# Performance work log

Hardware: AMD Instinct MI355X
Metric: run time of the kernel (lower is better)

The kernel has to match this reference:

```python
import jax, jax.numpy as jnp
import numpy as np

T, B, D, W = 1024, 8, 512, 32

def setup_inputs() -> dict:
    key = jax.random.key(0)
    k1, k2, k3 = jax.random.split(key, 3)
    inputs = jax.random.normal(k1, (T, B, D), dtype=jnp.float32)
    weight_W = jax.random.uniform(k2, (D, D), dtype=jnp.float32, minval=-0.1, maxval=0.1)
    weight_proj = jax.random.uniform(k3, (D, 1), dtype=jnp.float32, minval=-0.1, maxval=0.1)
    return {"inputs": inputs, "weight_W": weight_W, "weight_proj": weight_proj,
            "attention_width": W}

def reference(inputs, weight_W, weight_proj, attention_width):
    # inputs: [T, B, D]. For step i < w: passthrough. For i >= w: attend over
    # window inputs[i-w : i] (current step EXCLUDED, matching the original).
    Tn, Bn, Dn = inputs.shape
    w = attention_width
    # window gather indices: row t corresponds to output step i = t + w,
    # covering timesteps [i-w, i) == [t, t+w)
    idx = jnp.arange(Tn - w)[:, None] + jnp.arange(w)          # [T-w, w]
    windows = inputs[idx]                                       # [T-w, w, B, D]
    u = jnp.tanh(jnp.einsum('twbd,de->twbe', windows, weight_W))  # [T-w, w, B, D]
    scores = jnp.einsum('twbd,d->twb', u, weight_proj[:, 0])      # [T-w, w, B]
    # NOTE: original uses legacy nn.Softmax() on a [w, B] tensor, whose implicit
    # dim is 1 (the batch dim). We reproduce that math faithfully: softmax over B.
    a = jax.nn.softmax(scores, axis=-1)                           # [T-w, w, B]
    attended = jnp.einsum('twb,twbd->tbd', a, windows)            # [T-w, B, D]
    return jnp.concatenate([inputs[:w], attended], axis=0)       # [T, B, D]
```

## Files before the change

### kernel.cpp

```cpp
#include <hip/hip_runtime.h>
#include <cstdint>

namespace {
constexpr int T = 1024;
constexpr int B = 8;
constexpr int D = 512;
constexpr int W = 32;
constexpr int M = T * B;
}

using half8  = __attribute__((ext_vector_type(8))) _Float16;
using f32x16 = __attribute__((ext_vector_type(16))) float;

__device__ __forceinline__ void gload16(const void* g, void* l) {
    __builtin_amdgcn_global_load_lds(
        (const __attribute__((address_space(1))) void*)g,
        (__attribute__((address_space(3))) void*)l, 16, 0, 0);
}

__device__ __forceinline__ float fast_tanh(float x) {
    float e = __expf(2.f * x);
    return 1.f - 2.f / (e + 1.f);
}

__global__ __launch_bounds__(256) void prep_merged(
    const float* __restrict__ X, const float* __restrict__ Wm,
    _Float16* __restrict__ Ah, _Float16* __restrict__ Bt)
{
    __shared__ float tile[64][65];
    const int tid = threadIdx.x;
    const int bid = blockIdx.x;

    {
        const int c = bid * 256 + tid;
        const float4* X4 = reinterpret_cast<const float4*>(X);
        const float4 v0 = X4[(size_t)c * 2];
        const float4 v1 = X4[(size_t)c * 2 + 1];
        half8 h;
        h[0] = (_Float16)v0.x; h[1] = (_Float16)v0.y; h[2] = (_Float16)v0.z; h[3] = (_Float16)v0.w;
        h[4] = (_Float16)v1.x; h[5] = (_Float16)v1.y; h[6] = (_Float16)v1.z; h[7] = (_Float16)v1.w;
        *reinterpret_cast<half8*>(Ah + (size_t)c * 8) = h;
    }

    if (bid < 64) {
        const int bd = bid & 7;
        const int be = bid >> 3;
        const int r  = tid >> 2;
        const int c0 = (tid & 3) * 16;
        const float* src = Wm + (size_t)(be * 64 + r) * 512 + bd * 64 + c0;
#pragma unroll
        for (int j = 0; j < 16; j += 4) {
            const float4 v = *reinterpret_cast<const float4*>(src + j);
            tile[r][c0 + j]     = v.x;
            tile[r][c0 + j + 1] = v.y;
            tile[r][c0 + j + 2] = v.z;
            tile[r][c0 + j + 3] = v.w;
        }
        __syncthreads();
        const int dd = tid >> 2;
        const int e0 = (tid & 3) * 16;
        half8 h0, h1;
#pragma unroll
        for (int j = 0; j < 8; ++j)  h0[j] = (_Float16)tile[e0 + j][dd];
#pragma unroll
        for (int j = 0; j < 8; ++j)  h1[j] = (_Float16)tile[e0 + 8 + j][dd];
        _Float16* dst = Bt + (size_t)(bd * 64 + dd) * 512 + be * 64 + e0;
        *reinterpret_cast<half8*>(dst)     = h0;
        *reinterpret_cast<half8*>(dst + 8) = h1;
    }
}

__global__ __launch_bounds__(256) void gemm_scores(
    const _Float16* __restrict__ Ah, const _Float16* __restrict__ Bt,
    const float* __restrict__ proj, float* __restrict__ spart)
{
    __shared__ char lds_buf[49152];

    const int tid  = threadIdx.x;
    const int lane = tid & 63;
    const int wv   = tid >> 6;
    const int wm   = wv >> 1;
    const int wn   = wv & 1;
    const int hi   = lane >> 5;
    const int l31  = lane & 31;
    const int l7   = lane & 7;

    const int bid  = blockIdx.x;
    const int wgid = (bid & 7) * 64 + (bid >> 3);
    const int mb   = wgid >> 2;
    const int nb   = wgid & 3;
    const int m0   = mb * 64;
    const int n0   = nb * 128;

    const int wbase = __builtin_amdgcn_readfirstlane(tid & ~63);

    f32x16 acc0 = {}, acc1 = {};

    auto stage = [&](int bufi, int kt) {
        char* abase = lds_buf + bufi * 24576;
        char* bbase = abase + 8192;
        const int kbase = kt * 64;
#pragma unroll
        for (int i = 0; i < 2; ++i) {
            const int c   = i * 256 + tid;
            const int row = c >> 3;
            const int ch  = c & 7;
            const int koff = kbase + ((ch ^ (row & 7)) << 3);
            gload16(Ah + (size_t)(m0 + row) * 512 + koff,
                    abase + (size_t)(i * 256 + wbase) * 16);
        }
#pragma unroll
        for (int i = 0; i < 4; ++i) {
            const int c   = i * 256 + tid;
            const int row = c >> 3;
            const int ch  = c & 7;
            const int koff = kbase + ((ch ^ (row & 7)) << 3);
            gload16(Bt + (size_t)(n0 + row) * 512 + koff,
                    bbase + (size_t)(i * 256 + wbase) * 16);
        }
    };

    stage(0, 0);
    asm volatile("s_waitcnt vmcnt(0)" ::: "memory");
    __syncthreads();

    int cur = 0;
    const int rowA  = wm * 32 + l31;
    const int colB0 = wn * 64 + l31;
    const int colB1 = colB0 + 32;

    for (int kt = 0; kt < 8; ++kt) {
        if (kt < 7) stage(cur ^ 1, kt + 1);

        const char* Ab = lds_buf + cur * 24576;
        const char* Bb = Ab + 8192;

        half8 af[4], bf0[4], bf1[4];
#pragma unroll
        for (int s = 0; s < 4; ++s) {
            const int ch = ((2 * s + hi) ^ l7) << 4;
            af[s]  = *reinterpret_cast<const half8*>(Ab + rowA  * 128 + ch);
            bf0[s] = *reinterpret_cast<const half8*>(Bb + colB0 * 128 + ch);
            bf1[s] = *reinterpret_cast<const half8*>(Bb + colB1 * 128 + ch);
        }
        __builtin_amdgcn_s_setprio(1);
#pragma unroll
        for (int s = 0; s < 4; ++s) {
            acc0 = __builtin_amdgcn_mfma_f32_32x32x16_f16(af[s], bf0[s], acc0, 0, 0, 0);
            acc1 = __builtin_amdgcn_mfma_f32_32x32x16_f16(af[s], bf1[s], acc1, 0, 0, 0);
        }
        __builtin_amdgcn_s_setprio(0);

        if (kt < 7) asm volatile("s_waitcnt vmcnt(0)" ::: "memory");
        __syncthreads();
        cur ^= 1;
    }

    const float pj0 = proj[n0 + wn * 64 + l31];
    const float pj1 = proj[n0 + wn * 64 + 32 + l31];
    float* sp = spart + (size_t)(nb * 2 + wn) * M;

#pragma unroll
    for (int reg = 0; reg < 16; ++reg) {
        float v0 = fast_tanh(acc0[reg]) * pj0 + fast_tanh(acc1[reg]) * pj1;
#pragma unroll
        for (int msk = 1; msk < 32; msk <<= 1)
            v0 += __shfl_xor(v0, msk, 64);
        if (l31 == 0) {
            const int rl = (reg & 3) + 8 * (reg >> 2) + 4 * hi;
            sp[m0 + wm * 32 + rl] = v0;
        }
    }
}

__global__ __launch_bounds__(256) void attend_kernel(
    const float* __restrict__ X, const _Float16* __restrict__ Ah,
    const float* __restrict__ spart, float* __restrict__ out)
{
    __shared__ _Float16 W_lds[63 * 512];
    __shared__ float p_lds[64];

    const int bid = blockIdx.x;
    const int b   = bid & 7;
    const int ig  = bid >> 3;
    const int tid = threadIdx.x;

    if (ig == 0) {
        const float4* X4 = reinterpret_cast<const float4*>(X);
        float4* O4 = reinterpret_cast<float4*>(out);
        for (int idx = tid; idx < 32 * 128; idx += 256) {
            const int r = idx >> 7;
            const int c = idx & 127;
            const size_t off = (size_t)(r * 8 + b) * 128 + c;
            O4[off] = X4[off];
        }
        return;
    }

    const int i0   = ig * 32;
    const int tau0 = i0 - 32;
    const int lane = tid & 63;
    const int wbase = __builtin_amdgcn_readfirstlane(tid & ~63);

    {
        const _Float16* src = Ah + (size_t)(tau0 * 8 + b) * 512;
#pragma unroll
        for (int it = 0; it < 16; ++it) {
            const int cbase = it * 256 + wbase;
            if (cbase < 4032) {
                const int c  = cbase + lane;
                const int r  = c >> 6;
                const int ch = c & 63;
                gload16(src + (size_t)r * 4096 + ch * 8,
                        (char*)W_lds + (size_t)cbase * 16);
            }
        }
    }

    const int bj = tid & 7;
#pragma unroll
    for (int half = 0; half < 2; ++half) {
        const int lt = (tid >> 3) + half * 32;
        if (lt < 63) {
            float s = 0.f;
#pragma unroll
            for (int g = 0; g < 8; ++g)
                s += spart[(size_t)g * M + (size_t)(tau0 + lt) * 8 + bj];
            float mx = s;
#pragma unroll
            for (int msk = 1; msk < 8; msk <<= 1)
                mx = fmaxf(mx, __shfl_xor(mx, msk, 64));
            const float e = __expf(s - mx);
            float sum = e;
#pragma unroll
            for (int msk = 1; msk < 8; msk <<= 1)
                sum += __shfl_xor(sum, msk, 64);
            if (bj == b) p_lds[lt] = e / sum;
        }
    }

    asm volatile("s_waitcnt vmcnt(0)" ::: "memory");
    __syncthreads();

    const int rg = tid >> 6;

#pragma unroll 2
    for (int q = 0; q < 8; ++q) {
        const int i  = i0 + rg * 8 + q;
        const int lb = rg * 8 + q;
        float a0 = 0.f, a1 = 0.f, a2 = 0.f, a3 = 0.f;
        float a4 = 0.f, a5 = 0.f, a6 = 0.f, a7 = 0.f;
#pragma unroll 4
        for (int k = 0; k < 32; ++k) {
            const int lt = lb + k;
            const float pw = p_lds[lt];
            const half8 h = *reinterpret_cast<const half8*>(
                W_lds + (size_t)lt * 512 + lane * 8);
            a0 = fmaf(pw, (float)h[0], a0);
            a1 = fmaf(pw, (float)h[1], a1);
            a2 = fmaf(pw, (float)h[2], a2);
            a3 = fmaf(pw, (float)h[3], a3);
            a4 = fmaf(pw, (float)h[4], a4);
            a5 = fmaf(pw, (float)h[5], a5);
            a6 = fmaf(pw, (float)h[6], a6);
            a7 = fmaf(pw, (float)h[7], a7);
        }
        float4* O4 = reinterpret_cast<float4*>(
            out + (size_t)(i * 8 + b) * 512 + lane * 8);
        O4[0] = float4{a0, a1, a2, a3};
        O4[1] = float4{a4, a5, a6, a7};
    }
}

extern "C" void kernel_launch(void* const* d_in, const int* in_sizes, int n_in,
                              void* d_out, int out_size, void* d_ws, size_t ws_size,
                              hipStream_t stream)
{
    const float* X    = (const float*)d_in[0];
    const float* Wm   = (const float*)d_in[1];
    const float* proj = (const float*)d_in[2];
    float* out = (float*)d_out;

    _Float16* Ah   = (_Float16*)d_ws;
    _Float16* Bt   = Ah + (size_t)M * D;
    float*    sprt = (float*)(Bt + (size_t)D * D);

    prep_merged<<<2048, 256, 0, stream>>>(X, Wm, Ah, Bt);
    gemm_scores<<<512, 256, 0, stream>>>(Ah, Bt, proj, sprt);
    attend_kernel<<<(T / W) * B, 256, 0, stream>>>(X, Ah, sprt, out);
}
```

Baseline: 41.02 us.

## Split attend blocks in half, reuse window rows across outputs, pipeline GEMM waits

The attend kernel now launches twice as many blocks, each covering 16 output steps and a 47-row window instead of 32 steps and 63 rows. Each wavefront computes 4 consecutive outputs at once, so every LDS row read and fp16 conversion feeds up to 4 accumulators instead of being reloaded per output. In the GEMM, the wait after issuing the next stage becomes a partial vmcnt wait plus a barrier at the top of the loop, so prefetch loads can overlap the current tile's MFMAs. The costs are more register pressure from the 32 accumulators, extra window rows loaded in total across the split blocks, and a partial-wait count that must match the number of issued loads.

```diff
diff --git a/kernel.cpp b/kernel.cpp
--- a/kernel.cpp
+++ b/kernel.cpp
@@ -121,8 +121,6 @@
     };
 
     stage(0, 0);
-    asm volatile("s_waitcnt vmcnt(0)" ::: "memory");
-    __syncthreads();
 
     int cur = 0;
     const int rowA  = wm * 32 + l31;
@@ -130,7 +128,13 @@
     const int colB1 = colB0 + 32;
 
     for (int kt = 0; kt < 8; ++kt) {
-        if (kt < 7) stage(cur ^ 1, kt + 1);
+        if (kt < 7) {
+            stage(cur ^ 1, kt + 1);
+            asm volatile("s_waitcnt vmcnt(6)" ::: "memory");
+        } else {
+            asm volatile("s_waitcnt vmcnt(0)" ::: "memory");
+        }
+        __syncthreads();
 
         const char* Ab = lds_buf + cur * 24576;
         const char* Bb = Ab + 8192;
@@ -151,7 +155,6 @@
         }
         __builtin_amdgcn_s_setprio(0);
 
-        if (kt < 7) asm volatile("s_waitcnt vmcnt(0)" ::: "memory");
         __syncthreads();
         cur ^= 1;
     }
@@ -177,27 +180,29 @@
     const float* __restrict__ X, const _Float16* __restrict__ Ah,
     const float* __restrict__ spart, float* __restrict__ out)
 {
-    __shared__ _Float16 W_lds[63 * 512];
-    __shared__ float p_lds[64];
-
-    const int bid = blockIdx.x;
-    const int b   = bid & 7;
-    const int ig  = bid >> 3;
+    __shared__ char lds[49152];
+    _Float16* W_lds = reinterpret_cast<_Float16*>(lds);
+    float*    p_lds = reinterpret_cast<float*>(lds + 48128);
+
+    const int vb  = blockIdx.x;
     const int tid = threadIdx.x;
+    const int ih  = vb & 1;
+    const int b   = (vb >> 1) & 7;
+    const int ig  = vb >> 4;
+    const int i0  = ig * 32 + ih * 16;
 
     if (ig == 0) {
         const float4* X4 = reinterpret_cast<const float4*>(X);
         float4* O4 = reinterpret_cast<float4*>(out);
-        for (int idx = tid; idx < 32 * 128; idx += 256) {
+        for (int idx = tid; idx < 16 * 128; idx += 256) {
             const int r = idx >> 7;
             const int c = idx & 127;
-            const size_t off = (size_t)(r * 8 + b) * 128 + c;
+            const size_t off = (size_t)((i0 + r) * 8 + b) * 128 + c;
             O4[off] = X4[off];
         }
         return;
     }
 
-    const int i0   = ig * 32;
     const int tau0 = i0 - 32;
     const int lane = tid & 63;
     const int wbase = __builtin_amdgcn_readfirstlane(tid & ~63);
@@ -205,9 +210,9 @@
     {
         const _Float16* src = Ah + (size_t)(tau0 * 8 + b) * 512;
 #pragma unroll
-        for (int it = 0; it < 16; ++it) {
+        for (int it = 0; it < 12; ++it) {
             const int cbase = it * 256 + wbase;
-            if (cbase < 4032) {
+            if (cbase < 3008) {
                 const int c  = cbase + lane;
                 const int r  = c >> 6;
                 const int ch = c & 63;
@@ -221,7 +226,7 @@
 #pragma unroll
     for (int half = 0; half < 2; ++half) {
         const int lt = (tid >> 3) + half * 32;
-        if (lt < 63) {
+        if (lt < 47) {
             float s = 0.f;
 #pragma unroll
             for (int g = 0; g < 8; ++g)
@@ -243,32 +248,39 @@
     __syncthreads();
 
     const int rg = tid >> 6;
-
-#pragma unroll 2
-    for (int q = 0; q < 8; ++q) {
-        const int i  = i0 + rg * 8 + q;
-        const int lb = rg * 8 + q;
-        float a0 = 0.f, a1 = 0.f, a2 = 0.f, a3 = 0.f;
-        float a4 = 0.f, a5 = 0.f, a6 = 0.f, a7 = 0.f;
-#pragma unroll 4
-        for (int k = 0; k < 32; ++k) {
-            const int lt = lb + k;
-            const float pw = p_lds[lt];
-            const half8 h = *reinterpret_cast<const half8*>(
-                W_lds + (size_t)lt * 512 + lane * 8);
-            a0 = fmaf(pw, (float)h[0], a0);
-            a1 = fmaf(pw, (float)h[1], a1);
-            a2 = fmaf(pw, (float)h[2], a2);
-            a3 = fmaf(pw, (float)h[3], a3);
-            a4 = fmaf(pw, (float)h[4], a4);
-            a5 = fmaf(pw, (float)h[5], a5);
-            a6 = fmaf(pw, (float)h[6], a6);
-            a7 = fmaf(pw, (float)h[7], a7);
-        }
+    const int u0 = rg * 4;
+    float acc[4][8];
+#pragma unroll
+    for (int q = 0; q < 4; ++q)
+#pragma unroll
+        for (int j = 0; j < 8; ++j) acc[q][j] = 0.f;
+
+    auto apply = [&](int u, int qlo, int qhi) {
+        const int lt = u0 + u;
+        const float pw = p_lds[lt];
+        const half8 h = *reinterpret_cast<const half8*>(
+            W_lds + (size_t)lt * 512 + lane * 8);
+        float hf[8];
+#pragma unroll
+        for (int j = 0; j < 8; ++j) hf[j] = (float)h[j];
+        for (int q = qlo; q <= qhi; ++q)
+#pragma unroll
+            for (int j = 0; j < 8; ++j)
+                acc[q][j] = fmaf(pw, hf[j], acc[q][j]);
+    };
+
+#pragma unroll
+    for (int u = 0; u < 3; ++u)  apply(u, 0, u);
+    for (int u = 3; u < 32; ++u) apply(u, 0, 3);
+#pragma unroll
+    for (int u = 32; u < 35; ++u) apply(u, u - 31, 3);
+
+#pragma unroll
+    for (int q = 0; q < 4; ++q) {
         float4* O4 = reinterpret_cast<float4*>(
-            out + (size_t)(i * 8 + b) * 512 + lane * 8);
-        O4[0] = float4{a0, a1, a2, a3};
-        O4[1] = float4{a4, a5, a6, a7};
+            out + (size_t)((i0 + u0 + q) * 8 + b) * 512 + lane * 8);
+        O4[0] = float4{acc[q][0], acc[q][1], acc[q][2], acc[q][3]};
+        O4[1] = float4{acc[q][4], acc[q][5], acc[q][6], acc[q][7]};
     }
 }
 
@@ -287,5 +299,5 @@
 
     prep_merged<<<2048, 256, 0, stream>>>(X, Wm, Ah, Bt);
     gemm_scores<<<512, 256, 0, stream>>>(Ah, Bt, proj, sprt);
-    attend_kernel<<<(T / W) * B, 256, 0, stream>>>(X, Ah, sprt, out);
-}
+    attend_kernel<<<(T / W) * B * 2, 256, 0, stream>>>(X, Ah, sprt, out);
+}
```

New measurement: 36.79 us. -10.3%, faster.
